# Performance work log

Measured on AMD Instinct MI355X. Metric: run time of the kernel, lower is better.

## Reference

```python
import jax, jax.numpy as jnp
import numpy as np

N_NODES, N_HYPER, N_SEMA, D, L, E, NB = 100000, 20000, 10, 64, 2, 1000000, 50000
EPS = 1e-9


def setup_inputs() -> dict:
    key = jax.random.key(0)
    ks = jax.random.split(key, 20)
    s = 1.0 / np.sqrt(D)
    inp = {
        "node_emb": jax.random.normal(ks[0], (N_NODES, D), jnp.float32) * 0.1,
        "hyper_emb": jax.random.normal(ks[1], (N_HYPER, D), jnp.float32) * 0.1,
        "sema_emb": jax.random.normal(ks[2], (N_SEMA, D), jnp.float32) * 0.1,
        "W_msg": jax.random.normal(ks[3], (L, D, D), jnp.float32) * s,
        "W_att": jax.random.normal(ks[4], (L, D, D), jnp.float32) * s,
        "W_upd": jax.random.normal(ks[5], (L, D, D), jnp.float32) * s,
        "Wi1": jax.random.normal(ks[6], (L, D, D), jnp.float32) * s,
        "Wi2": jax.random.normal(ks[7], (L, D, D), jnp.float32) * s,
        "Wo_n": jax.random.normal(ks[8], (L, D, D), jnp.float32) * s,
        "Wo_e": jax.random.normal(ks[9], (L, D, D), jnp.float32) * s,
        "Wo_s": jax.random.normal(ks[10], (L, D, D), jnp.float32) * s,
        "node_indices": jax.random.randint(ks[11], (NB,), 0, N_NODES, jnp.int32),
        "hyperedge_indices": jax.random.randint(ks[12], (N_HYPER,), 0, N_HYPER, jnp.int32),
        "semalink_indices": jnp.arange(N_SEMA, dtype=jnp.int32),
        "semalinks": jnp.stack(
            [
                jax.random.randint(ks[13], (E,), 0, N_NODES, jnp.int32),
                jax.random.randint(ks[14], (E,), 0, N_HYPER, jnp.int32),
                jax.random.randint(ks[15], (E,), 0, N_SEMA, jnp.int32),
            ],
            axis=1,
        ),
    }
    return inp


def reference(node_emb, hyper_emb, sema_emb, W_msg, W_att, W_upd, Wi1, Wi2,
              Wo_n, Wo_e, Wo_s, node_indices, hyperedge_indices,
              semalink_indices, semalinks):
    N, d = node_emb.shape
    H = hyper_emb.shape[0]
    n_layers = W_msg.shape[0]

    # torch.isin(semalinks[:,0], node_indices) as a fixed-shape membership mask
    member = jnp.zeros((N,), bool).at[node_indices].set(True)
    src = semalinks[:, 0]   # node id per semalink
    hed = semalinks[:, 1]   # hyperedge id per semalink
    sem = semalinks[:, 2]   # semantic/relation id per semalink
    mask = member[src]      # [E] bool, replaces dynamic filtering
    maskf = mask.astype(node_emb.dtype)

    ne, he = node_emb, hyper_emb
    for i in range(n_layers):
        # --- SemalinkAttentiveAggregator: edge->hyperedge attentive scatter ---
        m = (ne[src] + sema_emb[sem]) @ W_msg[i]              # [E, d]
        q = he[hed] @ W_att[i]                                # [E, d]
        logits = jnp.where(mask, jnp.sum(m * q, axis=-1), -1e30)
        lmax = jax.ops.segment_max(logits, hed, num_segments=H)
        lmax = jnp.where(jnp.isfinite(lmax), lmax, 0.0)
        w = jnp.exp(logits - lmax[hed]) * maskf               # [E]
        denom = jax.ops.segment_sum(w, hed, num_segments=H)
        agg = jax.ops.segment_sum(w[:, None] * m, hed, num_segments=H)
        agg = agg / (denom[:, None] + EPS)
        new_he = jnp.tanh(agg @ W_upd[i])
        cnt_h = jax.ops.segment_sum(maskf, hed, num_segments=H)
        # scatter update: only hyperedges that received messages
        he = jnp.where((cnt_h > 0)[:, None], new_he, he)

        # --- InnerPropagation: node <- mean of incident hyperedges ---
        hmsg = he[hed] * maskf[:, None]                       # [E, d]
        n_sum = jax.ops.segment_sum(hmsg, src, num_segments=N)
        n_cnt = jax.ops.segment_sum(maskf, src, num_segments=N)
        n_agg = n_sum / (n_cnt[:, None] + EPS)                # [N, d]
        ne_inner = jax.nn.leaky_relu(ne @ Wi1[i] + n_agg @ Wi2[i])

        # --- OuterPropagation: relation-modulated hyperedge->node messages ---
        omsg = (he[hed] * sema_emb[sem]) * maskf[:, None]     # [E, d]
        o_agg = jax.ops.segment_sum(omsg, src, num_segments=N)
        o_agg = o_agg / (n_cnt[:, None] + EPS)
        ne = jnp.tanh(ne_inner @ Wo_n[i] + o_agg @ Wo_e[i] + n_agg @ Wo_s[i])

    # in-place scatter of updated minibatch node embeddings
    node_out = node_emb.at[node_indices].set(ne[node_indices])
    return node_out, he
```

## Files before the change

### kernel.cpp

```cpp
#include <hip/hip_runtime.h>
#include <cmath>


#define EPSF 1e-9f
#define NSLOT 40960
#define SENT 0xFFFFFFFFu
#define ATP 68
typedef unsigned long long ull;

__device__ __forceinline__ float group16_sum(float v){
  v += __shfl_xor(v, 1, 64);
  v += __shfl_xor(v, 2, 64);
  v += __shfl_xor(v, 4, 64);
  v += __shfl_xor(v, 8, 64);
  return v;
}
__device__ __forceinline__ float xgroup_sum(float v){
  v += __shfl_xor(v, 16, 64);
  v += __shfl_xor(v, 32, 64);
  return v;
}
__device__ __forceinline__ unsigned short f2bf(float f){
  unsigned b = __float_as_uint(f);
  unsigned r = (b + 0x7FFFu + ((b >> 16) & 1u)) >> 16;
  return (unsigned short)r;
}
__device__ __forceinline__ float bf2f(unsigned short u){
  return __uint_as_float(((unsigned)u) << 16);
}

__global__ __launch_bounds__(256) void k_copy4(const float4* __restrict__ in, float4* __restrict__ out, int n){
  int i = blockIdx.x*256 + threadIdx.x;
  if (i < n) out[i] = in[i];
}

__global__ __launch_bounds__(256) void k_set_member(const int* __restrict__ idx, int* __restrict__ member, int n){
  int i = blockIdx.x*256 + threadIdx.x;
  if (i < n) member[idx[i]] = 1;
}

__global__ __launch_bounds__(256) void k_build_list(int* __restrict__ member, int* __restrict__ mlist,
                                                    int* __restrict__ mcount, int N){
  int n = blockIdx.x*256 + threadIdx.x;
  if (n < N && member[n]) {
    int p = atomicAdd(mcount, 1);
    mlist[p] = n;
    member[n] = p + 2;
  }
}

__global__ __launch_bounds__(256) void k_count_rec(const int* __restrict__ sl, const int* __restrict__ member,
    ull* __restrict__ rec, ushort2* __restrict__ ranks,
    int* __restrict__ cnt_hed, int* __restrict__ cnt_slot, int E){
  int e = blockIdx.x*256 + threadIdx.x;
  if (e >= E) return;
  int src = sl[3*e];
  int m = member[src];
  if (m){
    int slot = m - 2;
    int hed = sl[3*e+1];
    int sem = sl[3*e+2];
    unsigned lo = (unsigned)slot | ((unsigned)sem << 20);
    rec[e] = (ull)lo | ((ull)(unsigned)hed << 32);
    int r1 = atomicAdd(&cnt_hed[hed], 1);
    int r2 = atomicAdd(&cnt_slot[slot], 1);
    ushort2 rk; rk.x = (unsigned short)r1; rk.y = (unsigned short)r2;
    ranks[e] = rk;
  } else {
    rec[e] = (ull)SENT << 32;
  }
}

__global__ __launch_bounds__(256) void k_scan1(const int* __restrict__ in, int* __restrict__ out, int n,
                                               int* __restrict__ partials){
  __shared__ int s[256];
  int b = blockIdx.x, t = threadIdx.x;
  int base = b*2048 + t*8;
  int v[8]; int sum = 0;
  #pragma unroll
  for (int j=0;j<8;j++){ int i = base + j; v[j] = (i<n) ? in[i] : 0; sum += v[j]; }
  s[t] = sum;
  __syncthreads();
  for (int o=1;o<256;o<<=1){
    int x = (t>=o) ? s[t-o] : 0;
    __syncthreads();
    s[t] += x;
    __syncthreads();
  }
  int excl = s[t] - sum;
  if (t == 255) partials[b] = s[255];
  int run = excl;
  #pragma unroll
  for (int j=0;j<8;j++){ int i = base + j; if (i<n) out[i] = run; run += v[j]; }
}

__global__ void k_scan2(int* __restrict__ partials, int nb, int* __restrict__ out, int n){
  if (threadIdx.x==0 && blockIdx.x==0){
    int run = 0;
    for (int i=0;i<nb;i++){ int x = partials[i]; partials[i] = run; run += x; }
    out[n] = run;
  }
}

__global__ __launch_bounds__(256) void k_scan3(int* __restrict__ out, const int* __restrict__ partials, int n){
  int i = blockIdx.x*256 + threadIdx.x;
  if (i < n) out[i] += partials[i >> 11];
}

__global__ __launch_bounds__(256) void k_scatter_both(const ull* __restrict__ rec,
    const ushort2* __restrict__ ranks, const int* __restrict__ mcountp,
    const int* __restrict__ off_hed, unsigned* __restrict__ edge_hed,
    const int* __restrict__ off_slot, unsigned* __restrict__ edge_src, int E){
  int w = blockIdx.x & 3;
  int chunk = blockIdx.x >> 2;
  int nchunk = gridDim.x >> 2;
  int per = (E + nchunk - 1) / nchunk;
  int lo_i = chunk * per;
  int hi_i = min(E, lo_i + per);
  int divs = (*mcountp + 3) >> 2;
  for (int i = lo_i + threadIdx.x; i < hi_i; i += 256){
    ull r = rec[i];
    unsigned hed = (unsigned)(r >> 32);
    if (hed == SENT) continue;
    unsigned lo = (unsigned)r;
    int slot = lo & 0xFFFFF;
    ushort2 rk = ranks[i];
    if ((int)hed / 5000 == w){
      edge_hed[off_hed[hed] + rk.x] = lo;
    }
    if (slot / divs == w){
      edge_src[off_slot[slot] + rk.y] = hed | (lo & 0xFFF00000u);
    }
  }
}

#define LOAD_W(Wl, Wsrc) for (int i_=threadIdx.x; i_<1024; i_+=256) ((float4*)Wl)[i_] = ((const float4*)(Wsrc))[i_];

#define STAGE_AT(At, ro, nrows, LOADEXPR)                              \
  {                                                                    \
    int cg_ = threadIdx.x & 15, rl_ = threadIdx.x >> 4;                \
    for (int p_ = 0; p_ < 4; ++p_){                                    \
      int rloc_ = p_*16 + rl_;                                         \
      int r_ = (ro) + rloc_;                                           \
      float4 v_ = make_float4(0.f,0.f,0.f,0.f);                        \
      if (r_ < (nrows)){ v_ = (LOADEXPR); }                            \
      At[cg_*4+0][rloc_] = v_.x;                                       \
      At[cg_*4+1][rloc_] = v_.y;                                       \
      At[cg_*4+2][rloc_] = v_.z;                                       \
      At[cg_*4+3][rloc_] = v_.w;                                       \
    }                                                                  \
  }

__device__ __forceinline__ void gemm44(const float* __restrict__ Wl, const float (*At)[ATP],
                                       int rg4, int cg4, float4 acc[4]){
  #pragma unroll 8
  for (int k = 0; k < 64; ++k){
    const float4 w = *(const float4*)&Wl[k*64 + cg4];
    const float4 a = *(const float4*)&At[k][rg4];
    acc[0].x = fmaf(a.x,w.x,acc[0].x); acc[0].y = fmaf(a.x,w.y,acc[0].y);
    acc[0].z = fmaf(a.x,w.z,acc[0].z); acc[0].w = fmaf(a.x,w.w,acc[0].w);
    acc[1].x = fmaf(a.y,w.x,acc[1].x); acc[1].y = fmaf(a.y,w.y,acc[1].y);
    acc[1].z = fmaf(a.y,w.z,acc[1].z); acc[1].w = fmaf(a.y,w.w,acc[1].w);
    acc[2].x = fmaf(a.z,w.x,acc[2].x); acc[2].y = fmaf(a.z,w.y,acc[2].y);
    acc[2].z = fmaf(a.z,w.z,acc[2].z); acc[2].w = fmaf(a.z,w.w,acc[2].w);
    acc[3].x = fmaf(a.w,w.x,acc[3].x); acc[3].y = fmaf(a.w,w.y,acc[3].y);
    acc[3].z = fmaf(a.w,w.z,acc[3].z); acc[3].w = fmaf(a.w,w.w,acc[3].w);
  }
}

#define ZERO4(a) { a[0]=make_float4(0,0,0,0); a[1]=make_float4(0,0,0,0); a[2]=make_float4(0,0,0,0); a[3]=make_float4(0,0,0,0); }

__global__ __launch_bounds__(256) void k_rowmatA(const float* __restrict__ ne, const float* __restrict__ Wm,
    const float* __restrict__ Wi1, const int* __restrict__ mlist, const int* __restrict__ mcountp,
    unsigned short* __restrict__ nm_bf, float* __restrict__ inner1){
  __shared__ float W1[4096], W2[4096];
  __shared__ float At[64][ATP];
  int t = threadIdx.x;
  int nrows = *mcountp;
  int ntiles = (nrows + 63) >> 6;
  LOAD_W(W1, Wm)
  LOAD_W(W2, Wi1)
  int cg4 = (t & 15)*4, rg4 = (t >> 4)*4;
  for (int tile = blockIdx.x; tile < ntiles; tile += gridDim.x){
    int ro = tile << 6;
    __syncthreads();
    STAGE_AT(At, ro, nrows, (*(const float4*)&ne[(size_t)mlist[r_]*64 + cg_*4]))
    __syncthreads();
    float4 a1[4]; ZERO4(a1)
    float4 a2[4]; ZERO4(a2)
    #pragma unroll 4
    for (int k = 0; k < 64; ++k){
      const float4 w1 = *(const float4*)&W1[k*64 + cg4];
      const float4 w2 = *(const float4*)&W2[k*64 + cg4];
      const float4 a  = *(const float4*)&At[k][rg4];
      a1[0].x=fmaf(a.x,w1.x,a1[0].x); a1[0].y=fmaf(a.x,w1.y,a1[0].y); a1[0].z=fmaf(a.x,w1.z,a1[0].z); a1[0].w=fmaf(a.x,w1.w,a1[0].w);
      a1[1].x=fmaf(a.y,w1.x,a1[1].x); a1[1].y=fmaf(a.y,w1.y,a1[1].y); a1[1].z=fmaf(a.y,w1.z,a1[1].z); a1[1].w=fmaf(a.y,w1.w,a1[1].w);
      a1[2].x=fmaf(a.z,w1.x,a1[2].x); a1[2].y=fmaf(a.z,w1.y,a1[2].y); a1[2].z=fmaf(a.z,w1.z,a1[2].z); a1[2].w=fmaf(a.z,w1.w,a1[2].w);
      a1[3].x=fmaf(a.w,w1.x,a1[3].x); a1[3].y=fmaf(a.w,w1.y,a1[3].y); a1[3].z=fmaf(a.w,w1.z,a1[3].z); a1[3].w=fmaf(a.w,w1.w,a1[3].w);
      a2[0].x=fmaf(a.x,w2.x,a2[0].x); a2[0].y=fmaf(a.x,w2.y,a2[0].y); a2[0].z=fmaf(a.x,w2.z,a2[0].z); a2[0].w=fmaf(a.x,w2.w,a2[0].w);
      a2[1].x=fmaf(a.y,w2.x,a2[1].x); a2[1].y=fmaf(a.y,w2.y,a2[1].y); a2[1].z=fmaf(a.y,w2.z,a2[1].z); a2[1].w=fmaf(a.y,w2.w,a2[1].w);
      a2[2].x=fmaf(a.z,w2.x,a2[2].x); a2[2].y=fmaf(a.z,w2.y,a2[2].y); a2[2].z=fmaf(a.z,w2.z,a2[2].z); a2[2].w=fmaf(a.z,w2.w,a2[2].w);
      a2[3].x=fmaf(a.w,w2.x,a2[3].x); a2[3].y=fmaf(a.w,w2.y,a2[3].y); a2[3].z=fmaf(a.w,w2.z,a2[3].z); a2[3].w=fmaf(a.w,w2.w,a2[3].w);
    }
    #pragma unroll
    for (int i = 0; i < 4; ++i){
      int r = ro + rg4 + i;
      if (r < nrows){
        ushort4 s;
        s.x = f2bf(a1[i].x); s.y = f2bf(a1[i].y); s.z = f2bf(a1[i].z); s.w = f2bf(a1[i].w);
        *(ushort4*)&nm_bf[(size_t)r*64 + cg4] = s;
        *(float4*)&inner1[(size_t)r*64 + cg4] = a2[i];
      }
    }
  }
}

__global__ __launch_bounds__(256) void k_rowmatB(const float* __restrict__ he, const float* __restrict__ sema,
    const float* __restrict__ Wa, const float* __restrict__ Wm,
    float* __restrict__ hq, float* __restrict__ smbuf, int H, int NS_){
  __shared__ float W1[4096];
  __shared__ float At[64][ATP];
  int t = threadIdx.x;
  if (blockIdx.x == 0 && t < 160){
    int sr = t >> 4, c4 = (t & 15)*4;
    float4 accs = make_float4(0,0,0,0);
    #pragma unroll 8
    for (int k = 0; k < 64; ++k){
      float a = sema[sr*64 + k];
      float4 w = *(const float4*)&Wm[k*64 + c4];
      accs.x = fmaf(a,w.x,accs.x); accs.y = fmaf(a,w.y,accs.y);
      accs.z = fmaf(a,w.z,accs.z); accs.w = fmaf(a,w.w,accs.w);
    }
    *(float4*)&smbuf[(size_t)sr*64 + c4] = accs;
  }
  LOAD_W(W1, Wa)
  int nrows = H;
  int ntiles = (nrows + 63) >> 6;
  int cg4 = (t & 15)*4, rg4 = (t >> 4)*4;
  for (int tile = blockIdx.x; tile < ntiles; tile += gridDim.x){
    int ro = tile << 6;
    __syncthreads();
    STAGE_AT(At, ro, nrows, (*(const float4*)&he[(size_t)r_*64 + cg_*4]))
    __syncthreads();
    float4 acc[4]; ZERO4(acc)
    gemm44(W1, At, rg4, cg4, acc);
    #pragma unroll
    for (int i = 0; i < 4; ++i){
      int r = ro + rg4 + i;
      if (r < nrows) *(float4*)&hq[(size_t)r*64 + cg4] = acc[i];
    }
  }
}

__global__ __launch_bounds__(256) void k_matfuse(const float* __restrict__ inner1, const float* __restrict__ nagg,
    const float* __restrict__ oagg, const float* __restrict__ Wi2, const float* __restrict__ Wn,
    const float* __restrict__ We, const float* __restrict__ Ws,
    const int* __restrict__ mlist, const int* __restrict__ mcountp, float* __restrict__ ne){
  __shared__ float Wl[4096];
  __shared__ float At[64][ATP];
  int t = threadIdx.x;
  int cnt = *mcountp;
  int ntiles = (cnt + 63) >> 6;
  int cg4 = (t & 15)*4, rg4 = (t >> 4)*4;
  for (int tile = blockIdx.x; tile < ntiles; tile += gridDim.x){
    int ro = tile << 6;
    __syncthreads();
    STAGE_AT(At, ro, cnt, (*(const float4*)&nagg[(size_t)r_*64 + cg_*4]))
    LOAD_W(Wl, Ws)
    __syncthreads();
    float4 acc[4]; ZERO4(acc)
    gemm44(Wl, At, rg4, cg4, acc);
    __syncthreads();
    LOAD_W(Wl, Wi2)
    __syncthreads();
    float4 p1[4]; ZERO4(p1)
    gemm44(Wl, At, rg4, cg4, p1);
    float x[4][4];
    #pragma unroll
    for (int i = 0; i < 4; ++i){
      int r = ro + rg4 + i;
      float4 v = make_float4(0.f,0.f,0.f,0.f);
      if (r < cnt) v = *(const float4*)&inner1[(size_t)r*64 + cg4];
      float x0 = p1[i].x + v.x, x1 = p1[i].y + v.y, x2 = p1[i].z + v.z, x3 = p1[i].w + v.w;
      x[i][0] = x0 >= 0.f ? x0 : 0.01f*x0;
      x[i][1] = x1 >= 0.f ? x1 : 0.01f*x1;
      x[i][2] = x2 >= 0.f ? x2 : 0.01f*x2;
      x[i][3] = x3 >= 0.f ? x3 : 0.01f*x3;
    }
    __syncthreads();
    #pragma unroll
    for (int i = 0; i < 4; ++i)
      #pragma unroll
      for (int j = 0; j < 4; ++j)
        At[cg4+j][rg4+i] = x[i][j];
    LOAD_W(Wl, Wn)
    __syncthreads();
    gemm44(Wl, At, rg4, cg4, acc);
    __syncthreads();
    STAGE_AT(At, ro, cnt, (*(const float4*)&oagg[(size_t)r_*64 + cg_*4]))
    LOAD_W(Wl, We)
    __syncthreads();
    gemm44(Wl, At, rg4, cg4, acc);
    #pragma unroll
    for (int i = 0; i < 4; ++i){
      int r = ro + rg4 + i;
      if (r < cnt){
        float4 o = make_float4(tanhf(acc[i].x), tanhf(acc[i].y), tanhf(acc[i].z), tanhf(acc[i].w));
        *(float4*)&ne[(size_t)mlist[r]*64 + cg4] = o;
      }
    }
  }
}

__global__ __launch_bounds__(256) void k_attn_upd(const int* __restrict__ off_hed, const unsigned* __restrict__ edge_hed,
    const unsigned short* __restrict__ nm_bf, const float* __restrict__ smb, const float* __restrict__ hq,
    const float* __restrict__ W, const float* __restrict__ he_cur, float* __restrict__ he_next,
    unsigned short* __restrict__ he_bf, int H){
  __shared__ float Wl[4096];
  __shared__ float sm_lds[640];
  __shared__ float aggl[256];
  int t = threadIdx.x;
  for (int i=t;i<1024;i+=256) ((float4*)Wl)[i] = ((const float4*)W)[i];
  for (int i=t;i<640;i+=256) sm_lds[i] = smb[i];
  __syncthreads();
  int w = t >> 6, lane = t & 63;
  int nhb = (H + 3) >> 2;
  for (int hb = blockIdx.x; hb < nhb; hb += gridDim.x){
    int h = hb*4 + w;
    if (h >= H) continue;
    int start = off_hed[h], end = off_hed[h+1];
    if (start == end){
      float v = he_cur[(size_t)h*64 + lane];
      he_next[(size_t)h*64 + lane] = v;
      he_bf[(size_t)h*64 + lane] = f2bf(v);
      continue;
    }
    int g = lane >> 4, dl = (lane & 15)*4;
    float4 q4 = *(const float4*)&hq[(size_t)h*64 + dl];
    float ax=0.f, ay=0.f, az=0.f, aw=0.f, dsum=0.f, m=-3.4e38f;
    for (int idx0 = start; idx0 < end; idx0 += 4){
      int idx = idx0 + g;
      bool valid = idx < end;
      unsigned u = valid ? edge_hed[idx] : 0u;
      int slot = u & 0xFFFFF, sem = u >> 20;
      float4 nm4 = make_float4(0.f,0.f,0.f,0.f);
      if (valid){
        ushort4 nu = *(const ushort4*)&nm_bf[(size_t)slot*64 + dl];
        nm4 = make_float4(bf2f(nu.x), bf2f(nu.y), bf2f(nu.z), bf2f(nu.w));
      }
      float4 sm4 = *(const float4*)&sm_lds[sem*64 + dl];
      float mkx = nm4.x+sm4.x, mky = nm4.y+sm4.y, mkz = nm4.z+sm4.z, mkw = nm4.w+sm4.w;
      float part = mkx*q4.x + mky*q4.y + mkz*q4.z + mkw*q4.w;
      part = group16_sum(part);
      float l = valid ? part : -3.4e38f;
      float mn = fmaxf(m, l);
      float scale = __expf(m - mn);
      float wgt = valid ? __expf(l - mn) : 0.f;
      ax = ax*scale + wgt*mkx; ay = ay*scale + wgt*mky;
      az = az*scale + wgt*mkz; aw = aw*scale + wgt*mkw;
      dsum = dsum*scale + wgt;
      m = mn;
    }
    float mg = fmaxf(m, __shfl_xor(m, 16, 64));
    mg = fmaxf(mg, __shfl_xor(mg, 32, 64));
    float cs = __expf(m - mg);
    ax*=cs; ay*=cs; az*=cs; aw*=cs; dsum*=cs;
    ax = xgroup_sum(ax); ay = xgroup_sum(ay); az = xgroup_sum(az); aw = xgroup_sum(aw);
    dsum = xgroup_sum(dsum);
    if (lane < 16){
      float inv = 1.f/(dsum + EPSF);
      aggl[w*64 + dl+0] = ax*inv;
      aggl[w*64 + dl+1] = ay*inv;
      aggl[w*64 + dl+2] = az*inv;
      aggl[w*64 + dl+3] = aw*inv;
    }
    float o = 0.f;
    #pragma unroll 8
    for (int j=0;j<64;j++) o = fmaf(aggl[w*64 + j], Wl[j*64 + lane], o);
    float ov = tanhf(o);
    he_next[(size_t)h*64 + lane] = ov;
    he_bf[(size_t)h*64 + lane] = f2bf(ov);
  }
}

__global__ __launch_bounds__(256) void k_nodeagg2(const int* __restrict__ mcountp,
    const int* __restrict__ off_slot, const unsigned* __restrict__ edge_src,
    const unsigned short* __restrict__ he_bf, const float* __restrict__ sema,
    float* __restrict__ nagg, float* __restrict__ oagg){
  __shared__ float sm_lds[640];
  int t = threadIdx.x;
  for (int i=t;i<640;i+=256) sm_lds[i] = sema[i];
  __syncthreads();
  int w = t >> 6, lane = t & 63;
  int mc = *mcountp;
  int npb = (mc + 3) >> 2;
  int g = lane >> 4, dl = (lane & 15)*4;
  for (int pb = blockIdx.x; pb < npb; pb += gridDim.x){
    int p = pb*4 + w;
    if (p >= mc) continue;
    int start = off_slot[p], end = off_slot[p+1];
    float anx=0.f, any_=0.f, anz=0.f, anw=0.f;
    float aox=0.f, aoy=0.f, aoz=0.f, aow=0.f;
    for (int idx0 = start; idx0 < end; idx0 += 4){
      int idx = idx0 + g;
      if (idx < end){
        unsigned u = edge_src[idx];
        int hd = u & 0xFFFFF, sem = u >> 20;
        ushort4 hu = *(const ushort4*)&he_bf[(size_t)hd*64 + dl];
        float4 hv = make_float4(bf2f(hu.x), bf2f(hu.y), bf2f(hu.z), bf2f(hu.w));
        float4 sv = *(const float4*)&sm_lds[sem*64 + dl];
        anx += hv.x; any_ += hv.y; anz += hv.z; anw += hv.w;
        aox = fmaf(hv.x, sv.x, aox); aoy = fmaf(hv.y, sv.y, aoy);
        aoz = fmaf(hv.z, sv.z, aoz); aow = fmaf(hv.w, sv.w, aow);
      }
    }
    anx = xgroup_sum(anx); any_ = xgroup_sum(any_); anz = xgroup_sum(anz); anw = xgroup_sum(anw);
    aox = xgroup_sum(aox); aoy = xgroup_sum(aoy); aoz = xgroup_sum(aoz); aow = xgroup_sum(aow);
    if (lane < 16){
      float inv = 1.f/((float)(end - start) + EPSF);
      *(float4*)&nagg[(size_t)p*64 + dl] = make_float4(anx*inv, any_*inv, anz*inv, anw*inv);
      *(float4*)&oagg[(size_t)p*64 + dl] = make_float4(aox*inv, aoy*inv, aoz*inv, aow*inv);
    }
  }
}

extern "C" void kernel_launch(void* const* d_in, const int* in_sizes, int n_in,
                              void* d_out, int out_size, void* d_ws, size_t ws_size,
                              hipStream_t stream)
{
  (void)in_sizes; (void)n_in; (void)out_size; (void)ws_size;
  const float* node_emb  = (const float*)d_in[0];
  const float* hyper_emb = (const float*)d_in[1];
  const float* sema_emb  = (const float*)d_in[2];
  const float* W_msg = (const float*)d_in[3];
  const float* W_att = (const float*)d_in[4];
  const float* W_upd = (const float*)d_in[5];
  const float* Wi1   = (const float*)d_in[6];
  const float* Wi2   = (const float*)d_in[7];
  const float* Wo_n  = (const float*)d_in[8];
  const float* Wo_e  = (const float*)d_in[9];
  const float* Wo_s  = (const float*)d_in[10];
  const int* node_indices = (const int*)d_in[11];
  const int* semalinks    = (const int*)d_in[14];

  constexpr int N = 100000, H = 20000, NS = 10, L = 2, E = 1000000, NB = 50000;

  float* out_ne = (float*)d_out;
  float* out_he = (float*)d_out + (size_t)N*64;

  char* wsp = (char*)d_ws;
  auto alloc = [&](size_t bytes)->char*{ char* p = wsp; wsp += (bytes + 255) & ~(size_t)255; return p; };
  char* zstart = wsp;
  int* member   = (int*)alloc((size_t)N*4);
  int* cnt_hed  = (int*)alloc((size_t)H*4);
  int* cnt_slot = (int*)alloc((size_t)NSLOT*4);
  int* mcount   = (int*)alloc(256);
  size_t zbytes = (size_t)(wsp - zstart);
  int* off_hed   = (int*)alloc((size_t)(H+1)*4);
  int* off_slot  = (int*)alloc((size_t)(NSLOT+1)*4);
  int* mlist     = (int*)alloc((size_t)NB*4);
  int* partials  = (int*)alloc(256);
  ull* rec       = (ull*)alloc((size_t)E*8);
  ushort2* ranks = (ushort2*)alloc((size_t)E*4);
  unsigned* edge_hed = (unsigned*)alloc((size_t)E*4);
  unsigned* edge_src = (unsigned*)alloc((size_t)E*4);
  float* smbuf  = (float*)alloc((size_t)NS*64*4);
  float* hq     = (float*)alloc((size_t)H*64*4);
  unsigned short* nm_bf = (unsigned short*)alloc((size_t)NB*64*2);
  unsigned short* he_bf = (unsigned short*)alloc((size_t)H*64*2);
  float* he1    = (float*)alloc((size_t)H*64*4);
  float* naggb  = (float*)alloc((size_t)NB*64*4);
  float* oaggb  = (float*)alloc((size_t)NB*64*4);
  float* inner1 = (float*)alloc((size_t)NB*64*4);

  hipMemsetAsync(zstart, 0, zbytes, stream);

  k_copy4<<<(N*64/4 + 255)/256, 256, 0, stream>>>((const float4*)node_emb, (float4*)out_ne, N*64/4);
  k_set_member<<<(NB+255)/256, 256, 0, stream>>>(node_indices, member, NB);
  k_build_list<<<(N+255)/256, 256, 0, stream>>>(member, mlist, mcount, N);
  k_count_rec<<<(E+255)/256, 256, 0, stream>>>(semalinks, member, rec, ranks, cnt_hed, cnt_slot, E);

  int nb_h = (H + 2047)/2048, nb_s = (NSLOT + 2047)/2048;
  k_scan1<<<nb_h, 256, 0, stream>>>(cnt_hed, off_hed, H, partials);
  k_scan2<<<1, 64, 0, stream>>>(partials, nb_h, off_hed, H);
  k_scan3<<<(H+255)/256, 256, 0, stream>>>(off_hed, partials, H);
  k_scan1<<<nb_s, 256, 0, stream>>>(cnt_slot, off_slot, NSLOT, partials);
  k_scan2<<<1, 64, 0, stream>>>(partials, nb_s, off_slot, NSLOT);
  k_scan3<<<(NSLOT+255)/256, 256, 0, stream>>>(off_slot, partials, NSLOT);

  k_scatter_both<<<2048, 256, 0, stream>>>(rec, ranks, mcount, off_hed, edge_hed,
                                           off_slot, edge_src, E);

  for (int i = 0; i < L; ++i){
    const float* Wm = W_msg + (size_t)i*4096;
    const float* Wa = W_att + (size_t)i*4096;
    const float* Wu = W_upd + (size_t)i*4096;
    const float* wi1 = Wi1 + (size_t)i*4096;
    const float* wi2 = Wi2 + (size_t)i*4096;
    const float* won = Wo_n + (size_t)i*4096;
    const float* woe = Wo_e + (size_t)i*4096;
    const float* wos = Wo_s + (size_t)i*4096;
    const float* he_cur = (i == 0) ? hyper_emb : he1;
    float* he_next = (i == 0) ? he1 : out_he;

    k_rowmatA<<<800, 256, 0, stream>>>(out_ne, Wm, wi1, mlist, mcount, nm_bf, inner1);
    k_rowmatB<<<320, 256, 0, stream>>>(he_cur, sema_emb, Wa, Wm, hq, smbuf, H, NS);
    k_attn_upd<<<2048, 256, 0, stream>>>(off_hed, edge_hed, nm_bf, smbuf, hq, Wu,
                                         he_cur, he_next, he_bf, H);
    k_nodeagg2<<<2048, 256, 0, stream>>>(mcount, off_slot, edge_src, he_bf, sema_emb, naggb, oaggb);
    k_matfuse<<<800, 256, 0, stream>>>(inner1, naggb, oaggb, wi2, won, woe, wos, mlist, mcount, out_ne);
  }
}
```

Measured before the change: 309.8 us.

## Pad atomic counters to separate cache lines and fuse embedding copy into count kernel

The per-hyperedge and per-slot atomic counters are spaced 16 ints apart (64 bytes) so that contended atomics on neighbouring counters stop sharing cache lines. The scan now reads them with a stride of 16. The node_emb to output copy, previously its own kernel, is folded into the edge counting kernel as a grid-stride loop that overlaps with the atomic-heavy work and saves a launch. In exchange the memset zeroes 16x more bytes for the counters and the scan reads are strided.

```diff
diff --git a/kernel.cpp b/kernel.cpp
--- a/kernel.cpp
+++ b/kernel.cpp
@@ -6,6 +6,7 @@
 #define NSLOT 40960
 #define SENT 0xFFFFFFFFu
 #define ATP 68
+#define CPAD 16
 typedef unsigned long long ull;
 
 __device__ __forceinline__ float group16_sum(float v){
@@ -27,11 +28,6 @@
 }
 __device__ __forceinline__ float bf2f(unsigned short u){
   return __uint_as_float(((unsigned)u) << 16);
-}
-
-__global__ __launch_bounds__(256) void k_copy4(const float4* __restrict__ in, float4* __restrict__ out, int n){
-  int i = blockIdx.x*256 + threadIdx.x;
-  if (i < n) out[i] = in[i];
 }
 
 __global__ __launch_bounds__(256) void k_set_member(const int* __restrict__ idx, int* __restrict__ member, int n){
@@ -51,23 +47,33 @@
 
 __global__ __launch_bounds__(256) void k_count_rec(const int* __restrict__ sl, const int* __restrict__ member,
     ull* __restrict__ rec, ushort2* __restrict__ ranks,
-    int* __restrict__ cnt_hed, int* __restrict__ cnt_slot, int E){
-  int e = blockIdx.x*256 + threadIdx.x;
-  if (e >= E) return;
-  int src = sl[3*e];
-  int m = member[src];
-  if (m){
-    int slot = m - 2;
-    int hed = sl[3*e+1];
-    int sem = sl[3*e+2];
-    unsigned lo = (unsigned)slot | ((unsigned)sem << 20);
-    rec[e] = (ull)lo | ((ull)(unsigned)hed << 32);
-    int r1 = atomicAdd(&cnt_hed[hed], 1);
-    int r2 = atomicAdd(&cnt_slot[slot], 1);
+    int* __restrict__ cnt_hed, int* __restrict__ cnt_slot, int E,
+    const float4* __restrict__ csrc, float4* __restrict__ cdst, int ncopy){
+  int gid = blockIdx.x*256 + threadIdx.x;
+  int e = gid;
+  bool valid = false;
+  int r1 = 0, r2 = 0;
+  if (e < E){
+    int src = sl[3*e];
+    int m = member[src];
+    if (m){
+      valid = true;
+      int slot = m - 2;
+      int hed = sl[3*e+1];
+      int sem = sl[3*e+2];
+      unsigned lo = (unsigned)slot | ((unsigned)sem << 20);
+      rec[e] = (ull)lo | ((ull)(unsigned)hed << 32);
+      r1 = atomicAdd(&cnt_hed[hed << 4], 1);
+      r2 = atomicAdd(&cnt_slot[slot << 4], 1);
+    } else {
+      rec[e] = (ull)SENT << 32;
+    }
+  }
+  int nthreads = gridDim.x * 256;
+  for (int i = gid; i < ncopy; i += nthreads) cdst[i] = csrc[i];
+  if (valid){
     ushort2 rk; rk.x = (unsigned short)r1; rk.y = (unsigned short)r2;
     ranks[e] = rk;
-  } else {
-    rec[e] = (ull)SENT << 32;
   }
 }
 
@@ -78,7 +84,7 @@
   int base = b*2048 + t*8;
   int v[8]; int sum = 0;
   #pragma unroll
-  for (int j=0;j<8;j++){ int i = base + j; v[j] = (i<n) ? in[i] : 0; sum += v[j]; }
+  for (int j=0;j<8;j++){ int i = base + j; v[j] = (i<n) ? in[(size_t)i << 4] : 0; sum += v[j]; }
   s[t] = sum;
   __syncthreads();
   for (int o=1;o<256;o<<=1){
@@ -452,8 +458,8 @@
   auto alloc = [&](size_t bytes)->char*{ char* p = wsp; wsp += (bytes + 255) & ~(size_t)255; return p; };
   char* zstart = wsp;
   int* member   = (int*)alloc((size_t)N*4);
-  int* cnt_hed  = (int*)alloc((size_t)H*4);
-  int* cnt_slot = (int*)alloc((size_t)NSLOT*4);
+  int* cnt_hed  = (int*)alloc((size_t)H*CPAD*4);
+  int* cnt_slot = (int*)alloc((size_t)NSLOT*CPAD*4);
   int* mcount   = (int*)alloc(256);
   size_t zbytes = (size_t)(wsp - zstart);
   int* off_hed   = (int*)alloc((size_t)(H+1)*4);
@@ -475,10 +481,10 @@
 
   hipMemsetAsync(zstart, 0, zbytes, stream);
 
-  k_copy4<<<(N*64/4 + 255)/256, 256, 0, stream>>>((const float4*)node_emb, (float4*)out_ne, N*64/4);
   k_set_member<<<(NB+255)/256, 256, 0, stream>>>(node_indices, member, NB);
   k_build_list<<<(N+255)/256, 256, 0, stream>>>(member, mlist, mcount, N);
-  k_count_rec<<<(E+255)/256, 256, 0, stream>>>(semalinks, member, rec, ranks, cnt_hed, cnt_slot, E);
+  k_count_rec<<<(E+255)/256, 256, 0, stream>>>(semalinks, member, rec, ranks, cnt_hed, cnt_slot, E,
+                                               (const float4*)node_emb, (float4*)out_ne, N*64/4);
 
   int nb_h = (H + 2047)/2048, nb_s = (NSLOT + 2047)/2048;
   k_scan1<<<nb_h, 256, 0, stream>>>(cnt_hed, off_hed, H, partials);
```

Result: faster. 302.8 us (-2.3%).
